# Optimization experiments

Hardware: AMD Instinct MI355X
Metric: run time of the kernel (lower is better)

The kernel has to match this reference:

```python
import jax, jax.numpy as jnp
import numpy as np

EPS = 1e-7  # K.epsilon()


def setup_inputs() -> dict:
    key = jax.random.key(0)
    k1, k2, k3, k4 = jax.random.split(key, 4)
    B, T, S = 64, 512, 1024
    x = jax.random.normal(k1, (B, T, S), dtype=jnp.float32)
    mask = jax.random.randint(k2, (B, T, S), 0, 2, dtype=jnp.int32)
    W = jax.random.normal(k3, (T, T), dtype=jnp.float32)
    b = jax.random.normal(k4, (T,), dtype=jnp.float32)
    return {"x": x, "mask": mask, "W": W, "b": b}


def reference(x, mask, W, b):
    # x: [B, T, S]; mask: [B, T, S] binary; W: [T, T]; b: [T]
    m = mask.astype(x.dtype)
    xp = jnp.swapaxes(x, 1, 2) * jnp.swapaxes(m, 1, 2)        # [B, S, T]
    z = jnp.tanh(jnp.einsum('bst,tu->bsu', xp, W) + b)        # [B, S, T]
    e = jnp.exp(z)
    att = e / (jnp.sum(e, axis=2, keepdims=True) + EPS)       # normalize over T
    # permute(att*xp) back to [B, T, S] then sum over S == sum over axis 1 here
    out = jnp.sum(att * xp, axis=1)                           # [B, T]
    return out
```

## Files before the change

kernel.cpp:

```cpp
#include <hip/hip_runtime.h>

typedef _Float16 half8 __attribute__((ext_vector_type(8)));
typedef float f32x4 __attribute__((ext_vector_type(4)));

#define LOG2E 1.44269504088896340736f


__device__ __forceinline__ void gll16(const void* g, void* l) {
    __builtin_amdgcn_global_load_lds(
        (const __attribute__((address_space(1))) unsigned int*)g,
        (__attribute__((address_space(3))) unsigned int*)l,
        16, 0, 0);
}

__global__ __launch_bounds__(256) void pack_w_kernel(const float* __restrict__ W,
                                                     uint4* __restrict__ wp) {
    __shared__ _Float16 sw[32][128];
    const int ks = blockIdx.x >> 2;
    const int nb = blockIdx.x & 3;
    const int tid = threadIdx.x;
    #pragma unroll
    for (int rep = 0; rep < 16; ++rep) {
        int idx = rep * 256 + tid;
        int k = idx >> 7, n = idx & 127;
        sw[k][n] = (_Float16)W[(size_t)(ks * 32 + k) * 512 + nb * 128 + n];
    }
    __syncthreads();
    #pragma unroll
    for (int rep = 0; rep < 2; ++rep) {
        int ci = rep * 256 + tid;
        int nloc = ci >> 2, q = ci & 3;
        int n = nb * 128 + nloc;
        int kb = q ^ (n & 3);
        union { _Float16 h[8]; uint4 u; } pk;
        #pragma unroll
        for (int j = 0; j < 8; ++j) pk.h[j] = sw[kb * 8 + j][nloc];
        wp[ks * 2048 + n * 4 + q] = pk.u;
    }
}

template <int USE_PACKED>
__global__ __launch_bounds__(256, 2)
void attn_fused_kernel(const float* __restrict__ x, const int* __restrict__ mask,
                       const float* __restrict__ Wraw, const uint4* __restrict__ wp4,
                       const float* __restrict__ bias, float* __restrict__ out) {
    __shared__ char sA[32768];
    __shared__ char sW[32768];

    const int tid  = threadIdx.x;
    const int lane = tid & 63;
    const int w    = tid >> 6;
    const int bid  = blockIdx.x;
    const int b    = bid >> 5;
    const int s0   = (bid & 31) * 32;
    const size_t xbase = (size_t)b * 512 * 1024;

    {
        const int sAi = lane & 31;
        const int p   = lane >> 5;
        #pragma unroll 8
        for (int it = 0; it < 32; ++it) {
            int t0 = w * 128 + it * 4 + p * 2;
            size_t g0 = xbase + (size_t)t0 * 1024 + s0 + sAi;
            float xv0 = x[g0];
            float xv1 = x[g0 + 1024];
            int   mv0 = mask[g0];
            int   mv1 = mask[g0 + 1024];
            float v0 = mv0 ? xv0 : 0.0f;
            float v1 = mv1 ? xv1 : 0.0f;
            _Float16 h0 = (_Float16)v0, h1 = (_Float16)v1;
            unsigned short u0, u1;
            __builtin_memcpy(&u0, &h0, 2);
            __builtin_memcpy(&u1, &h1, 2);
            unsigned pk = (unsigned)u0 | ((unsigned)u1 << 16);
            int byteoff = sAi * 1024 + ((((t0 >> 3) ^ sAi) & 63) << 4) + (t0 & 7) * 2;
            *((unsigned*)&sA[byteoff]) = pk;
        }
    }

    f32x4 acc[2][8];
    #pragma unroll
    for (int i = 0; i < 2; ++i)
        #pragma unroll
        for (int j2 = 0; j2 < 8; ++j2)
            acc[i][j2] = (f32x4){0.f, 0.f, 0.f, 0.f};

    for (int ks = 0; ks < 16; ++ks) {
        __syncthreads();
        if constexpr (USE_PACKED) {
            const uint4* src = wp4 + ks * 2048 + w * 512 + lane;
            char* dst = &sW[w * 8192];
            #pragma unroll
            for (int c = 0; c < 8; ++c)
                gll16(src + c * 64, dst + c * 1024);
        } else {
            #pragma unroll 4
            for (int rep = 0; rep < 64; ++rep) {
                int id = rep * 256 + tid;
                int n = id & 511, kk = id >> 9;
                float wv = Wraw[(size_t)(ks * 32 + kk) * 512 + n];
                _Float16 h = (_Float16)wv;
                int byteoff = (n * 4 + ((kk >> 3) ^ (n & 3))) * 16 + (kk & 7) * 2;
                *((_Float16*)&sW[byteoff]) = h;
            }
        }
        __syncthreads();

        half8 aF[2];
        #pragma unroll
        for (int mf = 0; mf < 2; ++mf) {
            int mA = mf * 16 + (lane & 15);
            int byteoff = mA * 1024 + (((ks * 4 + (lane >> 4)) ^ mA) << 4);
            aF[mf] = *((const half8*)&sA[byteoff]);
        }
        #pragma unroll
        for (int nf = 0; nf < 8; ++nf) {
            int n = w * 128 + nf * 16 + (lane & 15);
            int cchunk = n * 4 + ((lane >> 4) ^ (n & 3));
            half8 bF = *((const half8*)&sW[cchunk * 16]);
            acc[0][nf] = __builtin_amdgcn_mfma_f32_16x16x32_f16(aF[0], bF, acc[0][nf], 0, 0, 0);
            acc[1][nf] = __builtin_amdgcn_mfma_f32_16x16x32_f16(aF[1], bF, acc[1][nf], 0, 0, 0);
        }
    }

    float bb[8];
    #pragma unroll
    for (int nf = 0; nf < 8; ++nf)
        bb[nf] = bias[w * 128 + nf * 16 + (lane & 15)];

    float rs[2][4] = {};
    #pragma unroll
    for (int mf = 0; mf < 2; ++mf)
        #pragma unroll
        for (int nf = 0; nf < 8; ++nf)
            #pragma unroll
            for (int r = 0; r < 4; ++r) {
                float z = acc[mf][nf][r] + bb[nf];
                float u = __builtin_amdgcn_exp2f(z * (2.0f * LOG2E));
                float t = 1.0f - 2.0f * __builtin_amdgcn_rcpf(1.0f + u);
                float e = __builtin_amdgcn_exp2f(t * LOG2E);
                acc[mf][nf][r] = e;
                rs[mf][r] += e;
            }
    #pragma unroll
    for (int mf = 0; mf < 2; ++mf)
        #pragma unroll
        for (int r = 0; r < 4; ++r) {
            float v = rs[mf][r];
            v += __shfl_xor(v, 1);
            v += __shfl_xor(v, 2);
            v += __shfl_xor(v, 4);
            v += __shfl_xor(v, 8);
            rs[mf][r] = v;
        }
    __syncthreads();
    float* sc = (float*)sW;
    if ((lane & 15) == 0) {
        #pragma unroll
        for (int mf = 0; mf < 2; ++mf)
            #pragma unroll
            for (int r = 0; r < 4; ++r)
                sc[(mf * 16 + (lane >> 4) * 4 + r) * 4 + w] = rs[mf][r];
    }
    __syncthreads();
    float rcpden[2][4];
    #pragma unroll
    for (int mf = 0; mf < 2; ++mf)
        #pragma unroll
        for (int r = 0; r < 4; ++r) {
            int row = mf * 16 + (lane >> 4) * 4 + r;
            float d = sc[row * 4 + 0] + sc[row * 4 + 1] + sc[row * 4 + 2] + sc[row * 4 + 3] + 1e-7f;
            rcpden[mf][r] = __builtin_amdgcn_rcpf(d);
        }
    #pragma unroll
    for (int nf = 0; nf < 8; ++nf) {
        int n = w * 128 + nf * 16 + (lane & 15);
        float cs = 0.f;
        #pragma unroll
        for (int mf = 0; mf < 2; ++mf)
            #pragma unroll
            for (int r = 0; r < 4; ++r) {
                int row = mf * 16 + (lane >> 4) * 4 + r;
                float att = acc[mf][nf][r] * rcpden[mf][r];
                int byteoff = row * 1024 + ((((n >> 3) ^ row) & 63) << 4) + (n & 7) * 2;
                _Float16 hv = *((const _Float16*)&sA[byteoff]);
                cs += att * (float)hv;
            }
        cs += __shfl_xor(cs, 16);
        cs += __shfl_xor(cs, 32);
        if (lane < 16) atomicAdd(&out[b * 512 + n], cs);
    }
}

extern "C" void kernel_launch(void* const* d_in, const int* in_sizes, int n_in,
                              void* d_out, int out_size, void* d_ws, size_t ws_size,
                              hipStream_t stream) {
    const float* x    = (const float*)d_in[0];
    const int*   mask = (const int*)d_in[1];
    const float* W    = (const float*)d_in[2];
    const float* bias = (const float*)d_in[3];
    float* out = (float*)d_out;

    hipMemsetAsync(d_out, 0, (size_t)out_size * sizeof(float), stream);

    if (ws_size >= (size_t)524288) {
        uint4* wp = (uint4*)d_ws;
        pack_w_kernel<<<64, 256, 0, stream>>>(W, wp);
        attn_fused_kernel<1><<<2048, 256, 0, stream>>>(x, mask, W, wp, bias, out);
    } else {
        attn_fused_kernel<0><<<2048, 256, 0, stream>>>(x, mask, W, (const uint4*)nullptr, bias, out);
    }
}
```

Baseline: 345.1 us.

## Stream x/mask tiles per K-step with register prefetch instead of upfront staging

Instead of loading the whole 32x512 masked x slab into LDS before the GEMM loop, each K-step converts and stores only its 32-row slice, and prefetches the next slice into registers with float4/int4 loads. This overlaps global loads of x and mask with MFMA work and uses wider vector loads in place of scalar ones. The fp16 stores into LDS become scattered 2-byte writes, which may cause bank conflicts. The epilogue still reads the full slab, which is complete once the loop ends.

After: 316.1 us. -8.4%, faster.

```diff
diff --git a/kernel.cpp b/kernel.cpp
--- a/kernel.cpp
+++ b/kernel.cpp
@@ -55,28 +55,8 @@
     const int s0   = (bid & 31) * 32;
     const size_t xbase = (size_t)b * 512 * 1024;
 
-    {
-        const int sAi = lane & 31;
-        const int p   = lane >> 5;
-        #pragma unroll 8
-        for (int it = 0; it < 32; ++it) {
-            int t0 = w * 128 + it * 4 + p * 2;
-            size_t g0 = xbase + (size_t)t0 * 1024 + s0 + sAi;
-            float xv0 = x[g0];
-            float xv1 = x[g0 + 1024];
-            int   mv0 = mask[g0];
-            int   mv1 = mask[g0 + 1024];
-            float v0 = mv0 ? xv0 : 0.0f;
-            float v1 = mv1 ? xv1 : 0.0f;
-            _Float16 h0 = (_Float16)v0, h1 = (_Float16)v1;
-            unsigned short u0, u1;
-            __builtin_memcpy(&u0, &h0, 2);
-            __builtin_memcpy(&u1, &h1, 2);
-            unsigned pk = (unsigned)u0 | ((unsigned)u1 << 16);
-            int byteoff = sAi * 1024 + ((((t0 >> 3) ^ sAi) & 63) << 4) + (t0 & 7) * 2;
-            *((unsigned*)&sA[byteoff]) = pk;
-        }
-    }
+    const int tRow = tid >> 3;
+    const int m0   = (tid & 7) * 4;
 
     f32x4 acc[2][8];
     #pragma unroll
@@ -84,6 +64,15 @@
         #pragma unroll
         for (int j2 = 0; j2 < 8; ++j2)
             acc[i][j2] = (f32x4){0.f, 0.f, 0.f, 0.f};
+
+    float4 ax;
+    int4   am;
+    {
+        int t = tRow;
+        size_t g = xbase + (size_t)t * 1024 + s0 + m0;
+        ax = *reinterpret_cast<const float4*>(x + g);
+        am = *reinterpret_cast<const int4*>(mask + g);
+    }
 
     for (int ks = 0; ks < 16; ++ks) {
         __syncthreads();
@@ -104,13 +93,32 @@
                 *((_Float16*)&sW[byteoff]) = h;
             }
         }
+        {
+            int t = ks * 32 + tRow;
+            float xs[4] = {ax.x, ax.y, ax.z, ax.w};
+            int   ms[4] = {am.x, am.y, am.z, am.w};
+            #pragma unroll
+            for (int j = 0; j < 4; ++j) {
+                float v = ms[j] ? xs[j] : 0.0f;
+                _Float16 h = (_Float16)v;
+                int m = m0 + j;
+                int byteoff = m * 1024 + ((((t >> 3) ^ m) & 63) << 4) + (t & 7) * 2;
+                *((_Float16*)&sA[byteoff]) = h;
+            }
+        }
+        if (ks < 15) {
+            int t = (ks + 1) * 32 + tRow;
+            size_t g = xbase + (size_t)t * 1024 + s0 + m0;
+            ax = *reinterpret_cast<const float4*>(x + g);
+            am = *reinterpret_cast<const int4*>(mask + g);
+        }
         __syncthreads();
 
         half8 aF[2];
         #pragma unroll
         for (int mf = 0; mf < 2; ++mf) {
             int mA = mf * 16 + (lane & 15);
-            int byteoff = mA * 1024 + (((ks * 4 + (lane >> 4)) ^ mA) << 4);
+            int byteoff = mA * 1024 + ((((ks * 4 + (lane >> 4)) ^ mA) & 63) << 4);
             aF[mf] = *((const half8*)&sA[byteoff]);
         }
         #pragma unroll
```
